# Kernel optimization log

Hardware: AMD Instinct MI355X
Metric: run time of the kernel (lower is better)

## Reference

```python
import jax, jax.numpy as jnp
import numpy as np

N, B, T, E = 16384, 8, 32, 262144
D, H = 256, 8
HD = D // H

def _ln(x, g, b, eps=1e-5):
    m = x.mean(-1, keepdims=True)
    va = x.var(-1, keepdims=True)
    return (x - m) * jax.lax.rsqrt(va + eps) * g + b

def setup_inputs():
    key = jax.random.key(0)
    ks = jax.random.split(key, 40)
    rn = lambda i, sh, s=0.02: jax.random.normal(ks[i], sh, jnp.float32) * s
    inp = {}
    inp['x'] = jax.random.normal(ks[0], (N, D), jnp.float32)
    inp['edge_index'] = jax.random.randint(ks[1], (2, E), 0, N)
    inp['edge_attr'] = jax.random.normal(ks[2], (E, D), jnp.float32)
    inp['v'] = jax.random.normal(ks[3], (B, T, D), jnp.float32)
    inp['batch'] = jnp.sort(jax.random.randint(ks[4], (N,), 0, B))
    ones = lambda sh: jnp.ones(sh, jnp.float32)
    zeros = lambda sh: jnp.zeros(sh, jnp.float32)
    # LayerNorms
    inp['n1_g'], inp['n1_b'] = ones((D,)), zeros((D,))
    inp['vn_g'], inp['vn_b'] = ones((D,)), zeros((D,))
    inp['n3_g'], inp['n3_b'] = ones((D,)), zeros((D,))
    inp['n4_g'], inp['n4_b'] = ones((D,)), zeros((D,))
    # GINEConv: eps (train_eps, init 0) + MLP [D, 2D, D] with layer_norm+gelu on hidden
    inp['gine_eps'] = jnp.float32(0.0)
    inp['g_w1'], inp['g_b1'] = rn(5, (2 * D, D)), zeros((2 * D,))
    inp['g_lng'], inp['g_lnb'] = ones((2 * D,)), zeros((2 * D,))
    inp['g_w2'], inp['g_b2'] = rn(6, (D, 2 * D)), zeros((D,))
    # GatedResidual gammas (init 1e-5)
    inp['gamma1'] = jnp.full((D,), 1e-5, jnp.float32)
    inp['gamma2'] = jnp.full((D,), 1e-5, jnp.float32)
    inp['gamma3'] = jnp.full((D,), 1e-5, jnp.float32)
    # MultiheadAttention (packed in_proj)
    inp['mha_in_w'], inp['mha_in_b'] = rn(7, (3 * D, D)), zeros((3 * D,))
    inp['mha_out_w'], inp['mha_out_b'] = rn(8, (D, D)), zeros((D,))
    # node->token cross attention projections
    inp['q_w'], inp['q_b'] = rn(9, (D, D)), zeros((D,))
    inp['kv_w'], inp['kv_b'] = rn(10, (2 * D, D)), zeros((2 * D,))
    inp['o_w'], inp['o_b'] = rn(11, (D, D)), zeros((D,))
    # FFN MLP [D, 4D, D] (eval-mode batch_norm == identity with default stats)
    inp['f_w1'], inp['f_b1'] = rn(12, (4 * D, D)), zeros((4 * D,))
    inp['f_w2'], inp['f_b2'] = rn(13, (D, 4 * D)), zeros((D,))
    return inp

def reference(x, edge_index, edge_attr, v, batch,
              n1_g, n1_b, vn_g, vn_b, n3_g, n3_b, n4_g, n4_b,
              gine_eps, g_w1, g_b1, g_lng, g_lnb, g_w2, g_b2,
              gamma1, gamma2, gamma3,
              mha_in_w, mha_in_b, mha_out_w, mha_out_b,
              q_w, q_b, kv_w, kv_b, o_w, o_b,
              f_w1, f_b1, f_w2, f_b2):
    scale = HD ** -0.5
    gelu = lambda t: jax.nn.gelu(t, approximate=False)
    # --- GINEConv on norm1(x) ---
    xn = _ln(x, n1_g, n1_b)
    src, dst = edge_index[0], edge_index[1]
    msg = jax.nn.relu(xn[src] + edge_attr)                      # [E, D]
    agg = jax.ops.segment_sum(msg, dst, num_segments=N)         # [N, D]
    hin = (1.0 + gine_eps) * xn + agg
    h = gelu(_ln(hin @ g_w1.T + g_b1, g_lng, g_lnb)) @ g_w2.T + g_b2
    x = x + gamma1 * h                                          # res1 (drop_path off in eval)
    # --- token self-attention with node summary context ---
    v_res = v
    vn = _ln(v, vn_g, vn_b)
    cnt = jnp.maximum(jax.ops.segment_sum(jnp.ones((N,), x.dtype), batch, num_segments=B), 1.0)
    node_summary = jax.ops.segment_sum(x, batch, num_segments=B) / cnt[:, None]  # [B, D]
    ctx = jnp.concatenate([vn, node_summary[:, None, :]], axis=1)                # [B, T+1, D]
    wq, wk, wv = jnp.split(mha_in_w, 3, axis=0)
    bq, bk, bv = jnp.split(mha_in_b, 3, axis=0)
    qh = (vn @ wq.T + bq).reshape(B, T, H, HD)
    kh = (ctx @ wk.T + bk).reshape(B, T + 1, H, HD)
    vh = (ctx @ wv.T + bv).reshape(B, T + 1, H, HD)
    a = jax.nn.softmax(jnp.einsum('bqhd,bkhd->bhqk', qh, kh) * scale, axis=-1)
    v_upd = jnp.einsum('bhqk,bkhd->bqhd', a, vh).reshape(B, T, D) @ mha_out_w.T + mha_out_b
    v = v_res + gamma2 * v_upd                                  # res2
    # --- node -> token cross attention (gather-expand KV by batch) ---
    xn3 = _ln(x, n3_g, n3_b)
    q = (xn3 @ q_w.T + q_b).reshape(N, H, HD)
    kv = (v @ kv_w.T + kv_b).reshape(B, T, 2, H, HD)
    k, val = kv[:, :, 0], kv[:, :, 1]                           # [B, T, H, HD]
    k_exp, val_exp = k[batch], val[batch]                       # [N, T, H, HD]
    scores = jnp.einsum('nhd,nthd->nht', q, k_exp) * scale
    attn = jax.nn.softmax(scores, axis=-1)                      # scatter_softmax w/ all-zero idx == softmax over t
    attn_out = jnp.einsum('nht,nthd->nhd', attn, val_exp).reshape(N, D)
    x = x + gamma3 * (attn_out @ o_w.T + o_b)                   # res3
    # --- FFN ---
    xn4 = _ln(x, n4_g, n4_b)
    x = x + (gelu(xn4 @ f_w1.T + f_b1) @ f_w2.T + f_b2)
    return (x, v)
```

## Files before the change

kernel.cpp:

```cpp
#include <hip/hip_runtime.h>
#include <math.h>

#define NN 16384
#define EE 262144
#define BB 8
#define TT 32
#define DD 256
#define HH 8
#define HDD 32

typedef __bf16 bf16;
typedef __bf16 bf16x8 __attribute__((ext_vector_type(8)));
typedef __bf16 bf16x4 __attribute__((ext_vector_type(4)));
typedef float f32x4 __attribute__((ext_vector_type(4)));

#define GM_F32 0
#define GM_BF16 1
#define GM_GELU 2
#define GM_RES 3
#define GM_RES2 4

__device__ __forceinline__ float gelu_f(float v) {
  return 0.5f * v * (1.f + erff(v * 0.70710678118654752440f));
}

__device__ __forceinline__ void ln256w(const float* __restrict__ xr,
                                       const float* __restrict__ g,
                                       const float* __restrict__ bb,
                                       bf16* __restrict__ o) {
  int lane = threadIdx.x & 63;
  float4 v = *(const float4*)(xr + lane * 4);
  float s = v.x + v.y + v.z + v.w;
  float s2 = v.x * v.x + v.y * v.y + v.z * v.z + v.w * v.w;
#pragma unroll
  for (int off = 32; off > 0; off >>= 1) {
    s += __shfl_xor(s, off, 64);
    s2 += __shfl_xor(s2, off, 64);
  }
  float m = s * (1.f / 256.f);
  float rs = rsqrtf(s2 * (1.f / 256.f) - m * m + 1e-5f);
  float4 gg = *(const float4*)(g + lane * 4);
  float4 bv = *(const float4*)(bb + lane * 4);
  bf16x4 ov;
  ov[0] = (bf16)((v.x - m) * rs * gg.x + bv.x);
  ov[1] = (bf16)((v.y - m) * rs * gg.y + bv.y);
  ov[2] = (bf16)((v.z - m) * rs * gg.z + bv.z);
  ov[3] = (bf16)((v.w - m) * rs * gg.w + bv.w);
  *(bf16x4*)(o + lane * 4) = ov;
}

struct Pro {
  const float* wsrc[9];
  bf16* wdst[9];
// ... 38 lines not shown
  }
}

__global__ __launch_bounds__(1024) void scan16k(const int* __restrict__ deg,
                                                int* __restrict__ offs, int* __restrict__ woff) {
  __shared__ int part[1024];
  int t = threadIdx.x;
  int base = t * 16;
  int v[16];
  int s = 0;
#pragma unroll
  for (int j = 0; j < 16; ++j) { v[j] = deg[base + j]; s += v[j]; }
  part[t] = s;
  __syncthreads();
  for (int o = 1; o < 1024; o <<= 1) {
    int x = (t >= o) ? part[t - o] : 0;
    __syncthreads();
    part[t] += x;
    __syncthreads();
  }
  int excl = part[t] - s;
#pragma unroll
  for (int j = 0; j < 16; ++j) {
    offs[base + j] = excl;
    woff[base + j] = excl;
    excl += v[j];
  }
  if (t == 1023) offs[NN] = part[1023];
}

struct GemmP {
  const bf16* A; const bf16* W; const float* bias;
  int M, K, NC, mode;
  const float* res; const float* gamma;
  float* outf; bf16* outb;
};

__device__ __forceinline__ void gemm_core(const GemmP p, int bx, int by) {
  int wave = threadIdx.x >> 6;
  int lane = threadIdx.x & 63;
  int qd = lane >> 4;
  int l16 = lane & 15;
  int r0 = by * 128 + wave * 32;
  int c0 = bx * 64;
  int ar0 = r0 + l16;       if (ar0 >= p.M) ar0 = p.M - 1;
  int ar1 = r0 + 16 + l16;  if (ar1 >= p.M) ar1 = p.M - 1;
  const bf16* Ap0 = p.A + (size_t)ar0 * p.K + qd * 8;
  const bf16* Ap1 = p.A + (size_t)ar1 * p.K + qd * 8;
  const bf16* Wp = p.W + (size_t)(c0 + l16) * p.K + qd * 8;
  size_t K16 = (size_t)16 * p.K;
  f32x4 acc00 = {0.f, 0.f, 0.f, 0.f};
  f32x4 acc01 = acc00, acc02 = acc00, acc03 = acc00;
  f32x4 acc10 = acc00, acc11 = acc00, acc12 = acc00, acc13 = acc00;
  bf16x8 a0, a1, b0, b1, b2, b3, na0, na1, nb0, nb1, nb2, nb3;

#define GLOADS(A0, A1, B0, B1, B2, B3, kk)                \
  A0 = *(const bf16x8*)(Ap0 + (kk));                      \
  A1 = *(const bf16x8*)(Ap1 + (kk));                      \
  B0 = *(const bf16x8*)(Wp + (kk));                       \
  B1 = *(const bf16x8*)(Wp + K16 + (kk));                 \
  B2 = *(const bf16x8*)(Wp + 2 * K16 + (kk));             \
  B3 = *(const bf16x8*)(Wp + 3 * K16 + (kk));
#define GMFMAS(A0, A1, B0, B1, B2, B3)                                  \
  acc00 = __builtin_amdgcn_mfma_f32_16x16x32_bf16(A0, B0, acc00, 0, 0, 0); \
  acc01 = __builtin_amdgcn_mfma_f32_16x16x32_bf16(A0, B1, acc01, 0, 0, 0); \
  acc02 = __builtin_amdgcn_mfma_f32_16x16x32_bf16(A0, B2, acc02, 0, 0, 0); \
  acc03 = __builtin_amdgcn_mfma_f32_16x16x32_bf16(A0, B3, acc03, 0, 0, 0); \
  acc10 = __builtin_amdgcn_mfma_f32_16x16x32_bf16(A1, B0, acc10, 0, 0, 0); \
  acc11 = __builtin_amdgcn_mfma_f32_16x16x32_bf16(A1, B1, acc11, 0, 0, 0); \
  acc12 = __builtin_amdgcn_mfma_f32_16x16x32_bf16(A1, B2, acc12, 0, 0, 0); \
  acc13 = __builtin_amdgcn_mfma_f32_16x16x32_bf16(A1, B3, acc13, 0, 0, 0);

  GLOADS(a0, a1, b0, b1, b2, b3, 0)
  int k = 32;
  for (; k + 32 < p.K; k += 64) {
    GLOADS(na0, na1, nb0, nb1, nb2, nb3, k)
    GMFMAS(a0, a1, b0, b1, b2, b3)
    GLOADS(a0, a1, b0, b1, b2, b3, k + 32)
    GMFMAS(na0, na1, nb0, nb1, nb2, nb3)
  }
  GLOADS(na0, na1, nb0, nb1, nb2, nb3, k)
  GMFMAS(a0, a1, b0, b1, b2, b3)
  GMFMAS(na0, na1, nb0, nb1, nb2, nb3)
#undef GLOADS
#undef GMFMAS

  f32x4 accs[2][4] = {{acc00, acc01, acc02, acc03}, {acc10, acc11, acc12, acc13}};
#pragma unroll
  for (int s = 0; s < 2; ++s) {
#pragma unroll
    for (int c = 0; c < 4; ++c) {
      int col = c0 + c * 16 + l16;
      float bv = p.bias[col];
#pragma unroll
      for (int i = 0; i < 4; ++i) {
        int row = r0 + s * 16 + qd * 4 + i;
        if (row >= p.M) continue;
        size_t idx = (size_t)row * p.NC + col;
        float v = accs[s][c][i] + bv;
        if (p.mode == GM_F32) p.outf[idx] = v;
        else if (p.mode == GM_BF16) p.outb[idx] = (bf16)v;
        else if (p.mode == GM_GELU) p.outb[idx] = (bf16)gelu_f(v);
        else {
          float g = p.gamma ? p.gamma[col] : 1.f;
          float r = p.res[idx] + g * v;
          p.outf[idx] = r;
          if (p.mode == GM_RES2) p.outb[idx] = (bf16)r;
        }
      }
    }
  }
}

__global__ __launch_bounds__(256) void gemm_one(GemmP p, int nbx) {
  gemm_core(p, blockIdx.x % nbx, blockIdx.x / nbx);
}

__global__ __launch_bounds__(256) void csr_fill_qh(const int* __restrict__ ei,
                                                   int* __restrict__ woff,
                                                   int2* __restrict__ csr2, GemmP qp) {
  int b = blockIdx.x;
  if (b < 1024) {
    int e = b * 256 + threadIdx.x;
    int d = ei[EE + e];
    int s = ei[e];
    int p = atomicAdd(&woff[d], 1);
    csr2[p] = make_int2(e, s);
  } else {
    int l = b - 1024;
    gemm_core(qp, l % 4, l / 4);
  }
}

__global__ __launch_bounds__(256) void gine_agg(const float* __restrict__ eattr,
                                                const bf16* __restrict__ xn,
                                                const int* __restrict__ offs,
                                                const int2* __restrict__ csr2,
                                                const float* __restrict__ epsp,
                                                bf16* __restrict__ hin) {
  int wave = threadIdx.x >> 6, lane = threadIdx.x & 63;
  int n = blockIdx.x * 4 + wave;
  int s0 = offs[n], s1 = offs[n + 1];
  f32x4 acc = {0.f, 0.f, 0.f, 0.f};
  int i = s0;
  int2 es = (i < s1) ? csr2[i] : make_int2(0, 0);
  for (; i < s1; ++i) {
    int2 cur = es;
    if (i + 1 < s1) es = csr2[i + 1];
    float4 ea = *(const float4*)(eattr + (size_t)cur.x * DD + lane * 4);
    bf16x4 xv = *(const bf16x4*)(xn + (size_t)cur.y * DD + lane * 4);
    acc[0] += fmaxf((float)xv[0] + ea.x, 0.f);
    acc[1] += fmaxf((float)xv[1] + ea.y, 0.f);
    acc[2] += fmaxf((float)xv[2] + ea.z, 0.f);
    acc[3] += fmaxf((float)xv[3] + ea.w, 0.f);
  }
  bf16x4 xs = *(const bf16x4*)(xn + (size_t)n * DD + lane * 4);
  float e1 = 1.f + epsp[0];
  bf16x4 o;
#pragma unroll
  for (int j = 0; j < 4; ++j)
    o[j] = (bf16)(e1 * (float)xs[j] + acc[j]);
  *(bf16x4*)(hin + (size_t)n * DD + lane * 4) = o;
}

__global__ __launch_bounds__(256) void gemm_g1_ln(const bf16* __restrict__ A,
                                                  const bf16* __restrict__ W,
                                                  const float* __restrict__ bias,
                                                  const float* __restrict__ lng,
                                                  const float* __restrict__ lnb,
                                                  bf16* __restrict__ out) {
  __shared__ float ssum[4][32], ssum2[4][32], smm[32], smr[32];
  int w = threadIdx.x >> 6, lane = threadIdx.x & 63;
  int qd = lane >> 4, l16 = lane & 15;
  int r0 = blockIdx.x * 32;
  int c0 = w * 128;
  const bf16* Ap0 = A + (size_t)(r0 + l16) * 256 + qd * 8;
  const bf16* Ap1 = Ap0 + (size_t)16 * 256;
  const bf16* Wp = W + (size_t)(c0 + l16) * 256 + qd * 8;
  f32x4 z = {0.f, 0.f, 0.f, 0.f};
  f32x4 acc0[8], acc1[8];
#pragma unroll
  for (int cf = 0; cf < 8; ++cf) { acc0[cf] = z; acc1[cf] = z; }
  for (int k = 0; k < 256; k += 32) {
    bf16x8 a0 = *(const bf16x8*)(Ap0 + k);
    bf16x8 a1 = *(const bf16x8*)(Ap1 + k);
#pragma unroll
    for (int cf = 0; cf < 8; ++cf) {
      bf16x8 bv = *(const bf16x8*)(Wp + (size_t)cf * 16 * 256 + k);
      acc0[cf] = __builtin_amdgcn_mfma_f32_16x16x32_bf16(a0, bv, acc0[cf], 0, 0, 0);
      acc1[cf] = __builtin_amdgcn_mfma_f32_16x16x32_bf16(a1, bv, acc1[cf], 0, 0, 0);
    }
  }
#pragma unroll
  for (int cf = 0; cf < 8; ++cf) {
    float bv = bias[c0 + cf * 16 + l16];
#pragma unroll
    for (int i = 0; i < 4; ++i) { acc0[cf][i] += bv; acc1[cf][i] += bv; }
  }
#pragma unroll
  for (int s = 0; s < 2; ++s) {
#pragma unroll
    for (int i = 0; i < 4; ++i) {
      float ps = 0.f, ps2 = 0.f;
#pragma unroll
      for (int cf = 0; cf < 8; ++cf) {
        float v = s ? acc1[cf][i] : acc0[cf][i];
        ps += v; ps2 += v * v;
      }
#pragma unroll
      for (int off = 8; off > 0; off >>= 1) {
        ps += __shfl_down(ps, off, 16);
        ps2 += __shfl_down(ps2, off, 16);
      }
      if (l16 == 0) { int rib = s * 16 + qd * 4 + i; ssum[w][rib] = ps; ssum2[w][rib] = ps2; }
    }
  }
  __syncthreads();
  if (threadIdx.x < 32) {
    int rib = threadIdx.x;
    float S = ssum[0][rib] + ssum[1][rib] + ssum[2][rib] + ssum[3][rib];
    float S2 = ssum2[0][rib] + ssum2[1][rib] + ssum2[2][rib] + ssum2[3][rib];
    float m = S * (1.f / 512.f);
    smm[rib] = m;
    smr[rib] = rsqrtf(S2 * (1.f / 512.f) - m * m + 1e-5f);
  }
  __syncthreads();
#pragma unroll
  for (int s = 0; s < 2; ++s) {
#pragma unroll
    for (int cf = 0; cf < 8; ++cf) {
      int col = c0 + cf * 16 + l16;
      float g = lng[col], b = lnb[col];
#pragma unroll
      for (int i = 0; i < 4; ++i) {
        int rib = s * 16 + qd * 4 + i;
        float v = ((s ? acc1[cf][i] : acc0[cf][i]) - smm[rib]) * smr[rib] * g + b;
        out[(size_t)(r0 + rib) * 512 + col] = (bf16)gelu_f(v);
      }
    }
  }
}

struct ResLnP {
  const bf16* A; const bf16* W; const float* bias;
  const float* res; const float* gamma;
  float* resout; const float* lng; const float* lnb; bf16* lnout;
  int K; int seg; const int* batch; float* summary;
};

__global__ __launch_bounds__(256) void gemm_res_ln(ResLnP p) {
  __shared__ float ssum[4][32], ssum2[4][32], smm[32], smr[32];
  int w = threadIdx.x >> 6, lane = threadIdx.x & 63;
  int qd = lane >> 4, l16 = lane & 15;
  int r0 = blockIdx.x * 32;
  int c0 = w * 64;
  const bf16* Ap0 = p.A + (size_t)(r0 + l16) * p.K + qd * 8;
  const bf16* Ap1 = Ap0 + (size_t)16 * p.K;
  const bf16* Wp = p.W + (size_t)(c0 + l16) * p.K + qd * 8;
  size_t K16 = (size_t)16 * p.K;
  f32x4 z = {0.f, 0.f, 0.f, 0.f};
  f32x4 acc0[4], acc1[4];
#pragma unroll
  for (int cf = 0; cf < 4; ++cf) { acc0[cf] = z; acc1[cf] = z; }
  for (int k = 0; k < p.K; k += 32) {
    bf16x8 a0 = *(const bf16x8*)(Ap0 + k);
    bf16x8 a1 = *(const bf16x8*)(Ap1 + k);
#pragma unroll
    for (int cf = 0; cf < 4; ++cf) {
      bf16x8 bv = *(const bf16x8*)(Wp + cf * K16 + k);
      acc0[cf] = __builtin_amdgcn_mfma_f32_16x16x32_bf16(a0, bv, acc0[cf], 0, 0, 0);
      acc1[cf] = __builtin_amdgcn_mfma_f32_16x16x32_bf16(a1, bv, acc1[cf], 0, 0, 0);
    }
  }
  float rr0[4][4], rr1[4][4];
#pragma unroll
  for (int cf = 0; cf < 4; ++cf) {
    int col = c0 + cf * 16 + l16;
    float bv = p.bias[col], gm = p.gamma[col];
#pragma unroll
    for (int i = 0; i < 4; ++i) {
// ... 24 lines not shown
#pragma unroll
      for (int off = 8; off > 0; off >>= 1) {
        ps += __shfl_down(ps, off, 16);
        ps2 += __shfl_down(ps2, off, 16);
      }
      if (l16 == 0) { int rib = s * 16 + qd * 4 + i; ssum[w][rib] = ps; ssum2[w][rib] = ps2; }
    }
  }
  __syncthreads();
  if (threadIdx.x < 32) {
    int rib = threadIdx.x;
    float S = ssum[0][rib] + ssum[1][rib] + ssum[2][rib] + ssum[3][rib];
    float S2 = ssum2[0][rib] + ssum2[1][rib] + ssum2[2][rib] + ssum2[3][rib];
    float m = S * (1.f / 256.f);
    smm[rib] = m;
    smr[rib] = rsqrtf(S2 * (1.f / 256.f) - m * m + 1e-5f);
  }
  __syncthreads();
#pragma unroll
  for (int cf = 0; cf < 4; ++cf) {
    int col = c0 + cf * 16 + l16;
    float lg = p.lng[col], lb = p.lnb[col];
#pragma unroll
    for (int i = 0; i < 4; ++i) {
      {
        int rib = qd * 4 + i;
        p.lnout[(size_t)(r0 + rib) * 256 + col] =
            (bf16)((rr0[cf][i] - smm[rib]) * smr[rib] * lg + lb);
      }
      {
        int rib = 16 + qd * 4 + i;
        p.lnout[(size_t)(r0 + rib) * 256 + col] =
            (bf16)((rr1[cf][i] - smm[rib]) * smr[rib] * lg + lb);
      }
    }
  }
  if (p.seg) {
    int b0 = p.batch[r0], b31 = p.batch[r0 + 31];
    if (b0 == b31) {
#pragma unroll
      for (int cf = 0; cf < 4; ++cf) {
        float sl = 0.f;
#pragma unroll
        for (int i = 0; i < 4; ++i) sl += rr0[cf][i] + rr1[cf][i];
        sl += __shfl_xor(sl, 16, 64);
        sl += __shfl_xor(sl, 32, 64);
        if (qd == 0) atomicAdd(&p.summary[(size_t)b0 * 256 + c0 + cf * 16 + l16], sl);
      }
    } else {
#pragma unroll
      for (int cf = 0; cf < 4; ++cf) {
        int col = c0 + cf * 16 + l16;
#pragma unroll
        for (int i = 0; i < 4; ++i) {
          atomicAdd(&p.summary[(size_t)p.batch[r0 + qd * 4 + i] * 256 + col], rr0[cf][i]);
          atomicAdd(&p.summary[(size_t)p.batch[r0 + 16 + qd * 4 + i] * 256 + col], rr1[cf][i]);
        }
      }
    }
  }
}

__global__ __launch_bounds__(256) void gemm_ffn(const bf16* __restrict__ A,
                                                const bf16* __restrict__ W1,
                                                const float* __restrict__ b1,
                                                const bf16* __restrict__ W2,
                                                const float* __restrict__ b2,
                                                const float* __restrict__ res,
                                                float* __restrict__ outx) {
  __shared__ bf16 t_lds[32 * 1032];
  int w = threadIdx.x >> 6, lane = threadIdx.x & 63;
  int qd = lane >> 4, l16 = lane & 15;
  int r0 = blockIdx.x * 32;
  {
    int c0 = w * 256;
    const bf16* Ap0 = A + (size_t)(r0 + l16) * 256 + qd * 8;
    const bf16* Ap1 = Ap0 + (size_t)16 * 256;
    const bf16* Wp = W1 + (size_t)(c0 + l16) * 256 + qd * 8;
    f32x4 z = {0.f, 0.f, 0.f, 0.f};
    f32x4 acc0[16], acc1[16];
#pragma unroll
    for (int cf = 0; cf < 16; ++cf) { acc0[cf] = z; acc1[cf] = z; }
    for (int k = 0; k < 256; k += 32) {
      bf16x8 a0 = *(const bf16x8*)(Ap0 + k);
      bf16x8 a1 = *(const bf16x8*)(Ap1 + k);
#pragma unroll
      for (int cf = 0; cf < 16; ++cf) {
        bf16x8 bv = *(const bf16x8*)(Wp + (size_t)cf * 16 * 256 + k);
        acc0[cf] = __builtin_amdgcn_mfma_f32_16x16x32_bf16(a0, bv, acc0[cf], 0, 0, 0);
        acc1[cf] = __builtin_amdgcn_mfma_f32_16x16x32_bf16(a1, bv, acc1[cf], 0, 0, 0);
// ... 16 lines not shown
    int c2 = w * 64;
    const bf16* Wp2 = W2 + (size_t)(c2 + l16) * 1024 + qd * 8;
    const bf16* lp0 = t_lds + l16 * 1032 + qd * 8;
    const bf16* lp1 = t_lds + (16 + l16) * 1032 + qd * 8;
    f32x4 z = {0.f, 0.f, 0.f, 0.f};
    f32x4 acc0[4], acc1[4];
#pragma unroll
    for (int cf = 0; cf < 4; ++cf) { acc0[cf] = z; acc1[cf] = z; }
    for (int k = 0; k < 1024; k += 32) {
      bf16x8 a0 = *(const bf16x8*)(lp0 + k);
      bf16x8 a1 = *(const bf16x8*)(lp1 + k);
#pragma unroll
      for (int cf = 0; cf < 4; ++cf) {
        bf16x8 bv = *(const bf16x8*)(Wp2 + (size_t)cf * 16 * 1024 + k);
        acc0[cf] = __builtin_amdgcn_mfma_f32_16x16x32_bf16(a0, bv, acc0[cf], 0, 0, 0);
        acc1[cf] = __builtin_amdgcn_mfma_f32_16x16x32_bf16(a1, bv, acc1[cf], 0, 0, 0);
      }
    }
#pragma unroll
    for (int cf = 0; cf < 4; ++cf) {
      int col = c2 + cf * 16 + l16;
      float bv = b2[col];
#pragma unroll
      for (int i = 0; i < 4; ++i) {
        int row0 = r0 + qd * 4 + i, row1 = row0 + 16;
        size_t i0 = (size_t)row0 * 256 + col, i1 = (size_t)row1 * 256 + col;
        outx[i0] = res[i0] + acc0[cf][i] + bv;
        outx[i1] = res[i1] + acc1[cf][i] + bv;
      }
    }
  }
}

__global__ __launch_bounds__(256) void mid2(const float* __restrict__ summary,
                                            const float* __restrict__ cntf,
                                            const bf16* __restrict__ vn,
                                            bf16* __restrict__ ctx,
                                            GemmP qp) {
  int b = blockIdx.x, t = threadIdx.x;
  if (b < BB * (TT + 1)) {
    int bb = b / (TT + 1), k = b % (TT + 1);
    float val;
    if (k < TT) val = (float)vn[((size_t)(bb * TT + k)) * DD + t];
    else val = summary[(size_t)bb * DD + t] / fmaxf(cntf[bb], 1.f);
    ctx[(size_t)b * DD + t] = (bf16)val;
  } else {
    int l = b - BB * (TT + 1);
    gemm_core(qp, l % 4, l / 4);
  }
}

__global__ __launch_bounds__(256) void mha_small(const float* __restrict__ qh,
                                                 const float* __restrict__ kvh,
                                                 bf16* __restrict__ vatt) {
  int b = blockIdx.x;
  int h = threadIdx.x >> 5, qi = threadIdx.x & 31;
  const float scale = 0.17677669529663687f;
  float sc[TT + 1];
  float mx = -1e30f;
  const float* qp = qh + ((size_t)(b * TT + qi)) * DD + h * HDD;
#pragma unroll
  for (int k = 0; k < TT + 1; ++k) {
    const float* kp = kvh + ((size_t)(b * (TT + 1) + k)) * 512 + h * HDD;
    float s = 0.f;
#pragma unroll
    for (int d = 0; d < HDD; ++d) s += qp[d] * kp[d];
    s *= scale;
    sc[k] = s;
    mx = fmaxf(mx, s);
  }
  float sum = 0.f;
#pragma unroll
  for (int k = 0; k < TT + 1; ++k) {
    sc[k] = __expf(sc[k] - mx);
    sum += sc[k];
  }
  float inv = 1.f / sum;
#pragma unroll
  for (int d = 0; d < HDD; ++d) {
    float o = 0.f;
#pragma unroll
    for (int k = 0; k < TT + 1; ++k)
      o += sc[k] * kvh[((size_t)(b * (TT + 1) + k)) * 512 + 256 + h * HDD + d];
    vatt[((size_t)(b * TT + qi)) * DD + h * HDD + d] = (bf16)(o * inv);
  }
}

__global__ __launch_bounds__(256) void cross_attn(const bf16* __restrict__ qx,
                                                  const float* __restrict__ kvx,
                                                  const int* __restrict__ batch,
                                                  bf16* __restrict__ attnout) {
  __shared__ float v_lds[TT * DD];
  int tid = threadIdx.x;
  int n0 = blockIdx.x * 16;
  int b0 = batch[n0];
  for (int i = tid; i < TT * DD; i += 256) {
    int t = i >> 8, c = i & 255;
    v_lds[i] = kvx[((size_t)(b0 * TT + t)) * 512 + 256 + c];
  }
  int h = tid >> 5, lt = tid & 31;
  float kreg[HDD];
  {
    const float* kp = kvx + ((size_t)(b0 * TT + lt)) * 512 + h * HDD;
#pragma unroll
    for (int d = 0; d < HDD; ++d) kreg[d] = kp[d];
  }
  __syncthreads();
  const float scale = 0.17677669529663687f;
  for (int ni = 0; ni < 16; ++ni) {
    int n = n0 + ni;
    int b = batch[n];
    const bf16* qp = qx + (size_t)n * DD + h * HDD;
    float s = 0.f;
    if (b == b0) {
#pragma unroll
      for (int d = 0; d < HDD; ++d) s += (float)qp[d] * kreg[d];
    } else {
// ... 67 lines not shown
  const float* o_b = (const float*)d_in[32];
  const float* f_w1 = (const float*)d_in[33];
  const float* f_b1 = (const float*)d_in[34];
  const float* f_w2 = (const float*)d_in[35];
  const float* f_b2 = (const float*)d_in[36];

  float* out_x = (float*)d_out;
  float* out_v = (float*)d_out + (size_t)NN * DD;

  char* wsp = (char*)d_ws;
  size_t off = 0;
  auto alloc = [&](size_t bytes) -> void* {
    void* p = wsp + off;
    off += (bytes + 255) & ~(size_t)255;
    return p;
  };
  float* t1f = (float*)alloc(33554432);
  bf16* xn_bf = (bf16*)alloc(8388608);
  bf16* qx_bf = xn_bf;
  bf16* t1g_bf = (bf16*)alloc(16777216);
  float* x2f = (float*)t1g_bf;
  float* x1f = (float*)alloc(16777216);
  bf16* hin_bf = (bf16*)alloc(8388608);
  bf16* xn3_bf = hin_bf;
  bf16* att_bf = (bf16*)alloc(8388608);
  bf16* xn4_bf = att_bf;
  int* deg = (int*)alloc(NN * 4);
  float* summary = (float*)alloc(BB * DD * 4);
  float* cntf = (float*)alloc(BB * 4);
  int* offs = (int*)alloc((NN + 1) * 4);
  int* woff = (int*)alloc(NN * 4);
  int2* csr2 = (int2*)alloc((size_t)EE * 8);
  bf16* vn_bf = (bf16*)alloc(BB * TT * DD * 2);
  bf16* ctx_bf = (bf16*)alloc(BB * (TT + 1) * DD * 2);
  float* qhf = (float*)alloc(BB * TT * DD * 4);
  float* kvhf = (float*)alloc(BB * (TT + 1) * 512 * 4);
  bf16* vatt_bf = (bf16*)alloc(BB * TT * DD * 2);
  bf16* vout_bf = (bf16*)alloc(BB * TT * DD * 2);
  float* kvxf = (float*)alloc(BB * TT * 512 * 4);
  bf16* wbuf = (bf16*)alloc((size_t)1310720 * 2);
  (void)t1f;

  bf16* g_w1b = wbuf;
  bf16* g_w2b = g_w1b + 131072;
  bf16* mha_in_wb = g_w2b + 131072;
  bf16* q_wb = mha_in_wb + 196608;
  bf16* kv_wb = q_wb + 65536;
  bf16* o_wb = kv_wb + 131072;
  bf16* f_w1b = o_wb + 65536;
  bf16* f_w2b = f_w1b + 262144;
  bf16* mha_out_wb = f_w2b + 262144;

  hipMemsetAsync(deg, 0, NN * 4 + BB * DD * 4 + 256, stream);

  Pro pr;
  pr.wsrc[0] = g_w1; pr.wdst[0] = g_w1b;
  pr.wsrc[1] = g_w2; pr.wdst[1] = g_w2b;
  pr.wsrc[2] = mha_in_w; pr.wdst[2] = mha_in_wb;
  pr.wsrc[3] = mha_out_w; pr.wdst[3] = mha_out_wb;
  pr.wsrc[4] = q_w; pr.wdst[4] = q_wb;
  pr.wsrc[5] = kv_w; pr.wdst[5] = kv_wb;
  pr.wsrc[6] = o_w; pr.wdst[6] = o_wb;
  pr.wsrc[7] = f_w1; pr.wdst[7] = f_w1b;
  pr.wsrc[8] = f_w2; pr.wdst[8] = f_w2b;
  int bs[10] = {0, 128, 256, 448, 512, 576, 704, 768, 1024, 1280};
  for (int i = 0; i < 10; ++i) pr.wblk[i] = bs[i];
  pr.x = x; pr.n1_g = n1_g; pr.n1_b = n1_b; pr.xn = xn_bf;
  pr.v = v; pr.vn_g = vn_g; pr.vn_b = vn_b; pr.vn = vn_bf;
  pr.batch = batch; pr.cntf = cntf;
  pr.ei = ei; pr.deg = deg;
  prologue<<<6528, 256, 0, stream>>>(pr);

  scan16k<<<1, 1024, 0, stream>>>(deg, offs, woff);

  GemmP j_qh = {vn_bf, mha_in_wb, mha_in_b, BB * TT, 256, 256, GM_F32,
                nullptr, nullptr, qhf, nullptr};
  csr_fill_qh<<<1024 + 8, 256, 0, stream>>>(ei, woff, csr2, j_qh);

  gine_agg<<<NN / 4, 256, 0, stream>>>(eattr, xn_bf, offs, csr2, gine_eps, hin_bf);

  gemm_g1_ln<<<NN / 32, 256, 0, stream>>>(hin_bf, g_w1b, g_b1, g_lng, g_lnb, t1g_bf);

  ResLnP j_g2 = {t1g_bf, g_w2b, g_b2, x, gamma1, x1f, n3_g, n3_b, xn3_bf,
                 512, 1, batch, summary};
  gemm_res_ln<<<NN / 32, 256, 0, stream>>>(j_g2);

  GemmP j_q = {xn3_bf, q_wb, q_b, NN, 256, 256, GM_BF16, nullptr, nullptr, nullptr, qx_bf};
  mid2<<<BB * (TT + 1) + 512, 256, 0, stream>>>(summary, cntf, vn_bf, ctx_bf, j_q);

  GemmP j_kvh = {ctx_bf, mha_in_wb + (size_t)256 * 256, mha_in_b + 256, BB * (TT + 1), 256, 512,
                 GM_F32, nullptr, nullptr, kvhf, nullptr};
  gemm_one<<<24, 256, 0, stream>>>(j_kvh, 8);

  mha_small<<<BB, 256, 0, stream>>>(qhf, kvhf, vatt_bf);

  GemmP j_mo = {vatt_bf, mha_out_wb, mha_out_b, BB * TT, 256, 256, GM_RES2, v, gamma2, out_v, vout_bf};
  gemm_one<<<8, 256, 0, stream>>>(j_mo, 4);

  GemmP j_kv = {vout_bf, kv_wb, kv_b, BB * TT, 256, 512, GM_F32, nullptr, nullptr, kvxf, nullptr};
  gemm_one<<<16, 256, 0, stream>>>(j_kv, 8);

  cross_attn<<<NN / 16, 256, 0, stream>>>(qx_bf, kvxf, batch, att_bf);

  ResLnP j_o = {att_bf, o_wb, o_b, x1f, gamma3, x2f, n4_g, n4_b, xn4_bf,
                256, 0, nullptr, nullptr};
  gemm_res_ln<<<NN / 32, 256, 0, stream>>>(j_o);

  gemm_ffn<<<NN / 32, 256, 0, stream>>>(xn4_bf, f_w1b, f_b1, f_w2b, f_b2, x2f, out_x);
}
```

Baseline: 888.7 us.

## Fuse GINE MLP GEMMs via LDS and collapse token-side chain into one kernel

The two GINE MLP GEMMs (with hidden LayerNorm+GELU, then the residual, norm3 and segment-sum epilogue) are fused into one kernel. The 512-wide hidden activation stays in shared memory instead of round-tripping through global memory. The token-side chain (ctx build, KV projection, small MHA, out-projection with residual, KV projection for cross attention) is fused into 8 blocks that run alongside the node Q-projection GEMM blocks in one launch. This cuts several launches and intermediate buffers, at the cost of large LDS use per block, which may reduce occupancy. The csr_fill blocks are also reordered so the small GEMM blocks launch first.

```diff
diff --git a/kernel.cpp b/kernel.cpp
--- a/kernel.cpp
+++ b/kernel.cpp
@@ -16,9 +16,6 @@
 
 #define GM_F32 0
 #define GM_BF16 1
-#define GM_GELU 2
-#define GM_RES 3
-#define GM_RES2 4
 
 __device__ __forceinline__ float gelu_f(float v) {
   return 0.5f * v * (1.f + erff(v * 0.70710678118654752440f));
@@ -123,7 +120,6 @@
 struct GemmP {
   const bf16* A; const bf16* W; const float* bias;
   int M, K, NC, mode;
-  const float* res; const float* gamma;
   float* outf; bf16* outb;
 };
 
@@ -190,36 +186,24 @@
         size_t idx = (size_t)row * p.NC + col;
         float v = accs[s][c][i] + bv;
         if (p.mode == GM_F32) p.outf[idx] = v;
-        else if (p.mode == GM_BF16) p.outb[idx] = (bf16)v;
-        else if (p.mode == GM_GELU) p.outb[idx] = (bf16)gelu_f(v);
-        else {
-          float g = p.gamma ? p.gamma[col] : 1.f;
-          float r = p.res[idx] + g * v;
-          p.outf[idx] = r;
-          if (p.mode == GM_RES2) p.outb[idx] = (bf16)r;
-        }
-      }
-    }
-  }
-}
-
-__global__ __launch_bounds__(256) void gemm_one(GemmP p, int nbx) {
-  gemm_core(p, blockIdx.x % nbx, blockIdx.x / nbx);
+        else p.outb[idx] = (bf16)v;
+      }
+    }
+  }
 }
 
 __global__ __launch_bounds__(256) void csr_fill_qh(const int* __restrict__ ei,
                                                    int* __restrict__ woff,
                                                    int2* __restrict__ csr2, GemmP qp) {
   int b = blockIdx.x;
-  if (b < 1024) {
-    int e = b * 256 + threadIdx.x;
+  if (b < 8) {
+    gemm_core(qp, b % 4, b / 4);
+  } else {
+    int e = (b - 8) * 256 + threadIdx.x;
     int d = ei[EE + e];
     int s = ei[e];
     int p = atomicAdd(&woff[d], 1);
     csr2[p] = make_int2(e, s);
-  } else {
-    int l = b - 1024;
-    gemm_core(qp, l % 4, l / 4);
   }
 }
 
@@ -254,79 +238,197 @@
   *(bf16x4*)(hin + (size_t)n * DD + lane * 4) = o;
 }
 
-__global__ __launch_bounds__(256) void gemm_g1_ln(const bf16* __restrict__ A,
-                                                  const bf16* __restrict__ W,
-                                                  const float* __restrict__ bias,
-                                                  const float* __restrict__ lng,
-                                                  const float* __restrict__ lnb,
-                                                  bf16* __restrict__ out) {
+struct G12P {
+  const bf16* A; const bf16* W1; const float* b1;
+  const float* lng; const float* lnb;
+  const bf16* W2; const float* b2;
+  const float* res; const float* gamma;
+  float* resout; const float* n3g; const float* n3b; bf16* xn3;
+  const int* batch; float* summary;
+};
+
+__global__ __launch_bounds__(256) void gemm_g1g2(G12P p) {
+  __shared__ bf16 t_l[32 * 520];
   __shared__ float ssum[4][32], ssum2[4][32], smm[32], smr[32];
   int w = threadIdx.x >> 6, lane = threadIdx.x & 63;
   int qd = lane >> 4, l16 = lane & 15;
   int r0 = blockIdx.x * 32;
-  int c0 = w * 128;
-  const bf16* Ap0 = A + (size_t)(r0 + l16) * 256 + qd * 8;
-  const bf16* Ap1 = Ap0 + (size_t)16 * 256;
-  const bf16* Wp = W + (size_t)(c0 + l16) * 256 + qd * 8;
-  f32x4 z = {0.f, 0.f, 0.f, 0.f};
-  f32x4 acc0[8], acc1[8];
-#pragma unroll
-  for (int cf = 0; cf < 8; ++cf) { acc0[cf] = z; acc1[cf] = z; }
-  for (int k = 0; k < 256; k += 32) {
-    bf16x8 a0 = *(const bf16x8*)(Ap0 + k);
-    bf16x8 a1 = *(const bf16x8*)(Ap1 + k);
+  {
+    int c0 = w * 128;
+    const bf16* Ap0 = p.A + (size_t)(r0 + l16) * 256 + qd * 8;
+    const bf16* Ap1 = Ap0 + (size_t)16 * 256;
+    const bf16* Wp = p.W1 + (size_t)(c0 + l16) * 256 + qd * 8;
+    f32x4 z = {0.f, 0.f, 0.f, 0.f};
+    f32x4 acc0[8], acc1[8];
+#pragma unroll
+    for (int cf = 0; cf < 8; ++cf) { acc0[cf] = z; acc1[cf] = z; }
+    for (int k = 0; k < 256; k += 32) {
+      bf16x8 a0 = *(const bf16x8*)(Ap0 + k);
+      bf16x8 a1 = *(const bf16x8*)(Ap1 + k);
+#pragma unroll
+      for (int cf = 0; cf < 8; ++cf) {
+        bf16x8 bv = *(const bf16x8*)(Wp + (size_t)cf * 16 * 256 + k);
+        acc0[cf] = __builtin_amdgcn_mfma_f32_16x16x32_bf16(a0, bv, acc0[cf], 0, 0, 0);
+        acc1[cf] = __builtin_amdgcn_mfma_f32_16x16x32_bf16(a1, bv, acc1[cf], 0, 0, 0);
+      }
+    }
 #pragma unroll
     for (int cf = 0; cf < 8; ++cf) {
-      bf16x8 bv = *(const bf16x8*)(Wp + (size_t)cf * 16 * 256 + k);
-      acc0[cf] = __builtin_amdgcn_mfma_f32_16x16x32_bf16(a0, bv, acc0[cf], 0, 0, 0);
-      acc1[cf] = __builtin_amdgcn_mfma_f32_16x16x32_bf16(a1, bv, acc1[cf], 0, 0, 0);
-    }
-  }
-#pragma unroll
-  for (int cf = 0; cf < 8; ++cf) {
-    float bv = bias[c0 + cf * 16 + l16];
-#pragma unroll
-    for (int i = 0; i < 4; ++i) { acc0[cf][i] += bv; acc1[cf][i] += bv; }
-  }
-#pragma unroll
-  for (int s = 0; s < 2; ++s) {
-#pragma unroll
-    for (int i = 0; i < 4; ++i) {
-      float ps = 0.f, ps2 = 0.f;
+      float bv = p.b1[c0 + cf * 16 + l16];
+#pragma unroll
+      for (int i = 0; i < 4; ++i) { acc0[cf][i] += bv; acc1[cf][i] += bv; }
+    }
+#pragma unroll
+    for (int s = 0; s < 2; ++s) {
+#pragma unroll
+      for (int i = 0; i < 4; ++i) {
+        float ps = 0.f, ps2 = 0.f;
+#pragma unroll
+        for (int cf = 0; cf < 8; ++cf) {
+          float v = s ? acc1[cf][i] : acc0[cf][i];
+          ps += v; ps2 += v * v;
+        }
+#pragma unroll
+        for (int off = 8; off > 0; off >>= 1) {
+          ps += __shfl_down(ps, off, 16);
+          ps2 += __shfl_down(ps2, off, 16);
+        }
+        if (l16 == 0) { int rib = s * 16 + qd * 4 + i; ssum[w][rib] = ps; ssum2[w][rib] = ps2; }
+      }
+    }
+    __syncthreads();
+    if (threadIdx.x < 32) {
+      int rib = threadIdx.x;
+      float S = ssum[0][rib] + ssum[1][rib] + ssum[2][rib] + ssum[3][rib];
+      float S2 = ssum2[0][rib] + ssum2[1][rib] + ssum2[2][rib] + ssum2[3][rib];
+      float m = S * (1.f / 512.f);
+      smm[rib] = m;
+      smr[rib] = rsqrtf(S2 * (1.f / 512.f) - m * m + 1e-5f);
+    }
+    __syncthreads();
+#pragma unroll
+    for (int s = 0; s < 2; ++s) {
 #pragma unroll
       for (int cf = 0; cf < 8; ++cf) {
-        float v = s ? acc1[cf][i] : acc0[cf][i];
-        ps += v; ps2 += v * v;
-      }
-#pragma unroll
-      for (int off = 8; off > 0; off >>= 1) {
-        ps += __shfl_down(ps, off, 16);
-        ps2 += __shfl_down(ps2, off, 16);
-      }
-      if (l16 == 0) { int rib = s * 16 + qd * 4 + i; ssum[w][rib] = ps; ssum2[w][rib] = ps2; }
+        int col = c0 + cf * 16 + l16;
+        float g = p.lng[col], b = p.lnb[col];
+#pragma unroll
+        for (int i = 0; i < 4; ++i) {
+          int rib = s * 16 + qd * 4 + i;
+          float v = ((s ? acc1[cf][i] : acc0[cf][i]) - smm[rib]) * smr[rib] * g + b;
+          t_l[rib * 520 + col] = (bf16)gelu_f(v);
+        }
+      }
     }
   }
   __syncthreads();
-  if (threadIdx.x < 32) {
-    int rib = threadIdx.x;
-    float S = ssum[0][rib] + ssum[1][rib] + ssum[2][rib] + ssum[3][rib];
-    float S2 = ssum2[0][rib] + ssum2[1][rib] + ssum2[2][rib] + ssum2[3][rib];
-    float m = S * (1.f / 512.f);
-    smm[rib] = m;
-    smr[rib] = rsqrtf(S2 * (1.f / 512.f) - m * m + 1e-5f);
-  }
-  __syncthreads();
-#pragma unroll
-  for (int s = 0; s < 2; ++s) {
-#pragma unroll
-    for (int cf = 0; cf < 8; ++cf) {
+  {
+    int c0 = w * 64;
+    const bf16* lp0 = t_l + l16 * 520 + qd * 8;
+    const bf16* lp1 = t_l + (16 + l16) * 520 + qd * 8;
+    const bf16* Wp = p.W2 + (size_t)(c0 + l16) * 512 + qd * 8;
+    f32x4 z = {0.f, 0.f, 0.f, 0.f};
+    f32x4 acc0[4], acc1[4];
+#pragma unroll
+    for (int cf = 0; cf < 4; ++cf) { acc0[cf] = z; acc1[cf] = z; }
+    for (int k = 0; k < 512; k += 32) {
+      bf16x8 a0 = *(const bf16x8*)(lp0 + k);
+      bf16x8 a1 = *(const bf16x8*)(lp1 + k);
+#pragma unroll
+      for (int cf = 0; cf < 4; ++cf) {
+        bf16x8 bv = *(const bf16x8*)(Wp + (size_t)cf * 16 * 512 + k);
+        acc0[cf] = __builtin_amdgcn_mfma_f32_16x16x32_bf16(a0, bv, acc0[cf], 0, 0, 0);
+        acc1[cf] = __builtin_amdgcn_mfma_f32_16x16x32_bf16(a1, bv, acc1[cf], 0, 0, 0);
+      }
+    }
+    float rr0[4][4], rr1[4][4];
+#pragma unroll
+    for (int cf = 0; cf < 4; ++cf) {
       int col = c0 + cf * 16 + l16;
-      float g = lng[col], b = lnb[col];
+      float bv = p.b2[col], gm = p.gamma[col];
 #pragma unroll
       for (int i = 0; i < 4; ++i) {
-        int rib = s * 16 + qd * 4 + i;
-        float v = ((s ? acc1[cf][i] : acc0[cf][i]) - smm[rib]) * smr[rib] * g + b;
-        out[(size_t)(r0 + rib) * 512 + col] = (bf16)gelu_f(v);
+        {
+          int row = r0 + qd * 4 + i;
+          size_t idx = (size_t)row * 256 + col;
+          float r = p.res[idx] + gm * (acc0[cf][i] + bv);
+          p.resout[idx] = r; rr0[cf][i] = r;
+        }
+        {
+          int row = r0 + 16 + qd * 4 + i;
+          size_t idx = (size_t)row * 256 + col;
+          float r = p.res[idx] + gm * (acc1[cf][i] + bv);
+          p.resout[idx] = r; rr1[cf][i] = r;
+        }
+      }
+    }
+    __syncthreads();
+#pragma unroll
+    for (int s = 0; s < 2; ++s) {
+#pragma unroll
+      for (int i = 0; i < 4; ++i) {
+        float ps = 0.f, ps2 = 0.f;
+#pragma unroll
+        for (int cf = 0; cf < 4; ++cf) {
+          float v = s ? rr1[cf][i] : rr0[cf][i];
+          ps += v; ps2 += v * v;
+        }
+#pragma unroll
+        for (int off = 8; off > 0; off >>= 1) {
+          ps += __shfl_down(ps, off, 16);
+          ps2 += __shfl_down(ps2, off, 16);
+        }
+        if (l16 == 0) { int rib = s * 16 + qd * 4 + i; ssum[w][rib] = ps; ssum2[w][rib] = ps2; }
+      }
+    }
+    __syncthreads();
+    if (threadIdx.x < 32) {
+      int rib = threadIdx.x;
+      float S = ssum[0][rib] + ssum[1][rib] + ssum[2][rib] + ssum[3][rib];
+      float S2 = ssum2[0][rib] + ssum2[1][rib] + ssum2[2][rib] + ssum2[3][rib];
+      float m = S * (1.f / 256.f);
+      smm[rib] = m;
+      smr[rib] = rsqrtf(S2 * (1.f / 256.f) - m * m + 1e-5f);
+    }
+    __syncthreads();
+#pragma unroll
+    for (int cf = 0; cf < 4; ++cf) {
+      int col = c0 + cf * 16 + l16;
+      float lg = p.n3g[col], lb = p.n3b[col];
+#pragma unroll
+      for (int i = 0; i < 4; ++i) {
+        {
+          int rib = qd * 4 + i;
+          p.xn3[(size_t)(r0 + rib) * 256 + col] =
+              (bf16)((rr0[cf][i] - smm[rib]) * smr[rib] * lg + lb);
+        }
+        {
+          int rib = 16 + qd * 4 + i;
+          p.xn3[(size_t)(r0 + rib) * 256 + col] =
+              (bf16)((rr1[cf][i] - smm[rib]) * smr[rib] * lg + lb);
+        }
+      }
+    }
+    int b0 = p.batch[r0], b31 = p.batch[r0 + 31];
+    if (b0 == b31) {
+#pragma unroll
+      for (int cf = 0; cf < 4; ++cf) {
+        float sl = 0.f;
+#pragma unroll
+        for (int i = 0; i < 4; ++i) sl += rr0[cf][i] + rr1[cf][i];
+        sl += __shfl_xor(sl, 16, 64);
+        sl += __shfl_xor(sl, 32, 64);
+        if (qd == 0) atomicAdd(&p.summary[(size_t)b0 * 256 + c0 + cf * 16 + l16], sl);
+      }
+    } else {
+#pragma unroll
+      for (int cf = 0; cf < 4; ++cf) {
+        int col = c0 + cf * 16 + l16;
+#pragma unroll
+        for (int i = 0; i < 4; ++i) {
+          atomicAdd(&p.summary[(size_t)p.batch[r0 + qd * 4 + i] * 256 + col], rr0[cf][i]);
+          atomicAdd(&p.summary[(size_t)p.batch[r0 + 16 + qd * 4 + i] * 256 + col], rr1[cf][i]);
+        }
       }
     }
   }
@@ -336,7 +438,7 @@
   const bf16* A; const bf16* W; const float* bias;
   const float* res; const float* gamma;
   float* resout; const float* lng; const float* lnb; bf16* lnout;
-  int K; int seg; const int* batch; float* summary;
+  int K;
 };
 
 __global__ __launch_bounds__(256) void gemm_res_ln(ResLnP p) {
@@ -427,30 +529,6 @@
         int rib = 16 + qd * 4 + i;
         p.lnout[(size_t)(r0 + rib) * 256 + col] =
             (bf16)((rr1[cf][i] - smm[rib]) * smr[rib] * lg + lb);
-      }
-    }
-  }
-  if (p.seg) {
-    int b0 = p.batch[r0], b31 = p.batch[r0 + 31];
-    if (b0 == b31) {
-#pragma unroll
-      for (int cf = 0; cf < 4; ++cf) {
-        float sl = 0.f;
-#pragma unroll
-        for (int i = 0; i < 4; ++i) sl += rr0[cf][i] + rr1[cf][i];
-        sl += __shfl_xor(sl, 16, 64);
-        sl += __shfl_xor(sl, 32, 64);
-        if (qd == 0) atomicAdd(&p.summary[(size_t)b0 * 256 + c0 + cf * 16 + l16], sl);
-      }
-    } else {
-#pragma unroll
-      for (int cf = 0; cf < 4; ++cf) {
-        int col = c0 + cf * 16 + l16;
-#pragma unroll
-        for (int i = 0; i < 4; ++i) {
-          atomicAdd(&p.summary[(size_t)p.batch[r0 + qd * 4 + i] * 256 + col], rr0[cf][i]);
-          atomicAdd(&p.summary[(size_t)p.batch[r0 + 16 + qd * 4 + i] * 256 + col], rr1[cf][i]);
-        }
       }
     }
   }
@@ -533,57 +611,202 @@
   }
 }
 
-__global__ __launch_bounds__(256) void mid2(const float* __restrict__ summary,
-                                            const float* __restrict__ cntf,
-                                            const bf16* __restrict__ vn,
-                                            bf16* __restrict__ ctx,
-                                            GemmP qp) {
-  int b = blockIdx.x, t = threadIdx.x;
-  if (b < BB * (TT + 1)) {
-    int bb = b / (TT + 1), k = b % (TT + 1);
-    float val;
-    if (k < TT) val = (float)vn[((size_t)(bb * TT + k)) * DD + t];
-    else val = summary[(size_t)bb * DD + t] / fmaxf(cntf[bb], 1.f);
-    ctx[(size_t)b * DD + t] = (bf16)val;
-  } else {
-    int l = b - BB * (TT + 1);
+struct VtP {
+  const bf16* vn; const float* summary; const float* cntf; const float* qh;
+  const bf16* wkv_in; const float* bkv_in;
+  const bf16* wmo; const float* bmo;
+  const float* vres; const float* gamma2; float* outv;
+  const bf16* wkv2; const float* bkv2; float* kvx;
+};
+
+__global__ __launch_bounds__(256) void q_vtail(GemmP qp, VtP vt) {
+  __shared__ bf16 sl[25928];
+  int blk = blockIdx.x;
+  if (blk >= 8) {
+    int l = blk - 8;
     gemm_core(qp, l % 4, l / 4);
-  }
-}
-
-__global__ __launch_bounds__(256) void mha_small(const float* __restrict__ qh,
-                                                 const float* __restrict__ kvh,
-                                                 bf16* __restrict__ vatt) {
-  int b = blockIdx.x;
-  int h = threadIdx.x >> 5, qi = threadIdx.x & 31;
+    return;
+  }
+  int bb = blk;
+  int t = threadIdx.x;
+  int w = t >> 6, lane = t & 63, qd = lane >> 4, l16 = lane & 15;
+  bf16* ctx_l = sl;
+  bf16* kvh_l = sl + 8768;
+  bf16* vatt_l = sl;
+  bf16* vout_l = sl + 8768;
   const float scale = 0.17677669529663687f;
-  float sc[TT + 1];
-  float mx = -1e30f;
-  const float* qp = qh + ((size_t)(b * TT + qi)) * DD + h * HDD;
-#pragma unroll
-  for (int k = 0; k < TT + 1; ++k) {
-    const float* kp = kvh + ((size_t)(b * (TT + 1) + k)) * 512 + h * HDD;
-    float s = 0.f;
-#pragma unroll
-    for (int d = 0; d < HDD; ++d) s += qp[d] * kp[d];
-    s *= scale;
-    sc[k] = s;
-    mx = fmaxf(mx, s);
-  }
-  float sum = 0.f;
-#pragma unroll
-  for (int k = 0; k < TT + 1; ++k) {
-    sc[k] = __expf(sc[k] - mx);
-    sum += sc[k];
-  }
-  float inv = 1.f / sum;
-#pragma unroll
-  for (int d = 0; d < HDD; ++d) {
-    float o = 0.f;
-#pragma unroll
-    for (int k = 0; k < TT + 1; ++k)
-      o += sc[k] * kvh[((size_t)(b * (TT + 1) + k)) * 512 + 256 + h * HDD + d];
-    vatt[((size_t)(b * TT + qi)) * DD + h * HDD + d] = (bf16)(o * inv);
+
+  {
+    float cinv = 1.f / fmaxf(vt.cntf[bb], 1.f);
+    for (int r = 0; r < 33; ++r) {
+      float val;
+      if (r < 32) val = (float)vt.vn[((size_t)(bb * 32 + r)) * 256 + t];
+      else val = vt.summary[(size_t)bb * 256 + t] * cinv;
+      ctx_l[r * 264 + t] = (bf16)val;
+    }
+  }
+  __syncthreads();
+
+  {
+    const bf16* a0p = ctx_l + (l16 < 32 ? l16 : 32) * 264 + qd * 8;
+    const bf16* a1p = ctx_l + ((16 + l16) < 32 ? (16 + l16) : 32) * 264 + qd * 8;
+    const bf16* a2p = ctx_l + 32 * 264 + qd * 8;
+#pragma unroll
+    for (int sc = 0; sc < 2; ++sc) {
+      int c0 = w * 128 + sc * 64;
+      const bf16* Wp = vt.wkv_in + (size_t)(c0 + l16) * 256 + qd * 8;
+      f32x4 z = {0.f, 0.f, 0.f, 0.f};
+      f32x4 acc[3][4];
+#pragma unroll
+      for (int rg = 0; rg < 3; ++rg)
+#pragma unroll
+        for (int cf = 0; cf < 4; ++cf) acc[rg][cf] = z;
+      for (int k = 0; k < 256; k += 32) {
+        bf16x8 av0 = *(const bf16x8*)(a0p + k);
+        bf16x8 av1 = *(const bf16x8*)(a1p + k);
+        bf16x8 av2 = *(const bf16x8*)(a2p + k);
+#pragma unroll
+        for (int cf = 0; cf < 4; ++cf) {
+          bf16x8 bv = *(const bf16x8*)(Wp + (size_t)cf * 16 * 256 + k);
+          acc[0][cf] = __builtin_amdgcn_mfma_f32_16x16x32_bf16(av0, bv, acc[0][cf], 0, 0, 0);
+          acc[1][cf] = __builtin_amdgcn_mfma_f32_16x16x32_bf16(av1, bv, acc[1][cf], 0, 0, 0);
+          acc[2][cf] = __builtin_amdgcn_mfma_f32_16x16x32_bf16(av2, bv, acc[2][cf], 0, 0, 0);
+        }
+      }
+#pragma unroll
+      for (int cf = 0; cf < 4; ++cf) {
+        int col = c0 + cf * 16 + l16;
+        float bv = vt.bkv_in[col];
+#pragma unroll
+        for (int rg = 0; rg < 3; ++rg) {
+#pragma unroll
+          for (int i = 0; i < 4; ++i) {
+            int row = rg * 16 + qd * 4 + i;
+            if (row < 33) kvh_l[row * 520 + col] = (bf16)(acc[rg][cf][i] + bv);
+          }
+        }
+      }
+    }
+  }
+  __syncthreads();
+
+  {
+    int h = t >> 5, qi = t & 31;
+    float qreg[HDD];
+    const float* qp = vt.qh + ((size_t)(bb * TT + qi)) * DD + h * HDD;
+#pragma unroll
+    for (int d = 0; d < HDD; ++d) qreg[d] = qp[d];
+    float sc[TT + 1];
+    float mx = -1e30f;
+#pragma unroll
+    for (int k = 0; k < TT + 1; ++k) {
+      float s = 0.f;
+#pragma unroll
+      for (int d = 0; d < HDD; ++d) s += qreg[d] * (float)kvh_l[k * 520 + h * HDD + d];
+      s *= scale;
+      sc[k] = s;
+      mx = fmaxf(mx, s);
+    }
+    float sum = 0.f;
+#pragma unroll
+    for (int k = 0; k < TT + 1; ++k) {
+      sc[k] = __expf(sc[k] - mx);
+      sum += sc[k];
+    }
+    float inv = 1.f / sum;
+#pragma unroll
+    for (int d = 0; d < HDD; ++d) {
+      float o = 0.f;
+#pragma unroll
+      for (int k = 0; k < TT + 1; ++k)
+        o += sc[k] * (float)kvh_l[k * 520 + 256 + h * HDD + d];
+      vatt_l[qi * 264 + h * HDD + d] = (bf16)(o * inv);
+    }
+  }
+  __syncthreads();
+
+  {
+    int c0 = w * 64;
+    const bf16* a0p = vatt_l + l16 * 264 + qd * 8;
+    const bf16* a1p = vatt_l + (16 + l16) * 264 + qd * 8;
+    const bf16* Wp = vt.wmo + (size_t)(c0 + l16) * 256 + qd * 8;
+    f32x4 z = {0.f, 0.f, 0.f, 0.f};
+    f32x4 acc0[4], acc1[4];
+#pragma unroll
+    for (int cf = 0; cf < 4; ++cf) { acc0[cf] = z; acc1[cf] = z; }
+    for (int k = 0; k < 256; k += 32) {
+      bf16x8 a0 = *(const bf16x8*)(a0p + k);
+      bf16x8 a1 = *(const bf16x8*)(a1p + k);
+#pragma unroll
+      for (int cf = 0; cf < 4; ++cf) {
+        bf16x8 bv = *(const bf16x8*)(Wp + (size_t)cf * 16 * 256 + k);
+        acc0[cf] = __builtin_amdgcn_mfma_f32_16x16x32_bf16(a0, bv, acc0[cf], 0, 0, 0);
+        acc1[cf] = __builtin_amdgcn_mfma_f32_16x16x32_bf16(a1, bv, acc1[cf], 0, 0, 0);
+      }
+    }
+#pragma unroll
+    for (int cf = 0; cf < 4; ++cf) {
+      int col = c0 + cf * 16 + l16;
+      float bv = vt.bmo[col], gm = vt.gamma2[col];
+#pragma unroll
+      for (int i = 0; i < 4; ++i) {
+        {
+          int row = qd * 4 + i;
+          size_t idx = (size_t)(bb * TT + row) * 256 + col;
+          float r = vt.vres[idx] + gm * (acc0[cf][i] + bv);
+          vt.outv[idx] = r;
+          vout_l[row * 264 + col] = (bf16)r;
+        }
+        {
+          int row = 16 + qd * 4 + i;
+          size_t idx = (size_t)(bb * TT + row) * 256 + col;
+          float r = vt.vres[idx] + gm * (acc1[cf][i] + bv);
+          vt.outv[idx] = r;
+          vout_l[row * 264 + col] = (bf16)r;
+        }
+      }
+    }
+  }
+  __syncthreads();
+
+  {
+    const bf16* a0p = vout_l + l16 * 264 + qd * 8;
+    const bf16* a1p = vout_l + (16 + l16) * 264 + qd * 8;
+#pragma unroll
+    for (int sc = 0; sc < 2; ++sc) {
+      int c0 = w * 128 + sc * 64;
+      const bf16* Wp = vt.wkv2 + (size_t)(c0 + l16) * 256 + qd * 8;
+      f32x4 z = {0.f, 0.f, 0.f, 0.f};
+      f32x4 acc0[4], acc1[4];
+#pragma unroll
+      for (int cf = 0; cf < 4; ++cf) { acc0[cf] = z; acc1[cf] = z; }
+      for (int k = 0; k < 256; k += 32) {
+        bf16x8 a0 = *(const bf16x8*)(a0p + k);
+        bf16x8 a1 = *(const bf16x8*)(a1p + k);
+#pragma unroll
+        for (int cf = 0; cf < 4; ++cf) {
+          bf16x8 bv = *(const bf16x8*)(Wp + (size_t)cf * 16 * 256 + k);
+          acc0[cf] = __builtin_amdgcn_mfma_f32_16x16x32_bf16(a0, bv, acc0[cf], 0, 0, 0);
+          acc1[cf] = __builtin_amdgcn_mfma_f32_16x16x32_bf16(a1, bv, acc1[cf], 0, 0, 0);
+        }
+      }
+#pragma unroll
+      for (int cf = 0; cf < 4; ++cf) {
+        int col = c0 + cf * 16 + l16;
+        float bv = vt.bkv2[col];
+#pragma unroll
+        for (int i = 0; i < 4; ++i) {
+          {
+            int row = qd * 4 + i;
+            vt.kvx[(size_t)(bb * TT + row) * 512 + col] = acc0[cf][i] + bv;
+          }
+          {
+            int row = 16 + qd * 4 + i;
+            vt.kvx[(size_t)(bb * TT + row) * 512 + col] = acc1[cf][i] + bv;
+          }
+        }
+      }
+    }
   }
 }
 
@@ -717,11 +940,7 @@
   int* woff = (int*)alloc(NN * 4);
   int2* csr2 = (int2*)alloc((size_t)EE * 8);
   bf16* vn_bf = (bf16*)alloc(BB * TT * DD * 2);
-  bf16* ctx_bf = (bf16*)alloc(BB * (TT + 1) * DD * 2);
   float* qhf = (float*)alloc(BB * TT * DD * 4);
-  float* kvhf = (float*)alloc(BB * (TT + 1) * 512 * 4);
-  bf16* vatt_bf = (bf16*)alloc(BB * TT * DD * 2);
-  bf16* vout_bf = (bf16*)alloc(BB * TT * DD * 2);
   float* kvxf = (float*)alloc(BB * TT * 512 * 4);
   bf16* wbuf = (bf16*)alloc((size_t)1310720 * 2);
   (void)t1f;
@@ -758,37 +977,27 @@
 
   scan16k<<<1, 1024, 0, stream>>>(deg, offs, woff);
 
-  GemmP j_qh = {vn_bf, mha_in_wb, mha_in_b, BB * TT, 256, 256, GM_F32,
-                nullptr, nullptr, qhf, nullptr};
+  GemmP j_qh = {vn_bf, mha_in_wb, mha_in_b, BB * TT, 256, 256, GM_F32, qhf, nullptr};
   csr_fill_qh<<<1024 + 8, 256, 0, stream>>>(ei, woff, csr2, j_qh);
 
   gine_agg<<<NN / 4, 256, 0, stream>>>(eattr, xn_bf, offs, csr2, gine_eps, hin_bf);
 
-  gemm_g1_ln<<<NN / 32, 256, 0, stream>>>(hin_bf, g_w1b, g_b1, g_lng, g_lnb, t1g_bf);
-
-  ResLnP j_g2 = {t1g_bf, g_w2b, g_b2, x, gamma1, x1f, n3_g, n3_b, xn3_bf,
-                 512, 1, batch, summary};
-  gemm_res_ln<<<NN / 32, 256, 0, stream>>>(j_g2);
-
-  GemmP j_q = {xn3_bf, q_wb, q_b, NN, 256, 256, GM_BF16, nullptr, nullptr, nullptr, qx_bf};
-  mid2<<<BB * (TT + 1) + 512, 256, 0, stream>>>(summary, cntf, vn_bf, ctx_bf, j_q);
-
-  GemmP j_kvh = {ctx_bf, mha_in_wb + (size_t)256 * 256, mha_in_b + 256, BB * (TT + 1), 256, 512,
-                 GM_F32, nullptr, nullptr, kvhf, nullptr};
-  gemm_one<<<24, 256, 0, stream>>>(j_kvh, 8);
-
-  mha_small<<<BB, 256, 0, stream>>>(qhf, kvhf, vatt_bf);
-
-  GemmP j_mo = {vatt_bf, mha_out_wb, mha_out_b, BB * TT, 256, 256, GM_RES2, v, gamma2, out_v, vout_bf};
-  gemm_one<<<8, 256, 0, stream>>>(j_mo, 4);
-
-  GemmP j_kv = {vout_bf, kv_wb, kv_b, BB * TT, 256, 512, GM_F32, nullptr, nullptr, kvxf, nullptr};
-  gemm_one<<<16, 256, 0, stream>>>(j_kv, 8);
+  G12P jg = {hin_bf, g_w1b, g_b1, g_lng, g_lnb, g_w2b, g_b2, x, gamma1,
+             x1f, n3_g, n3_b, xn3_bf, batch, summary};
+  gemm_g1g2<<<NN / 32, 256, 0, stream>>>(jg);
+
+  GemmP j_q = {xn3_bf, q_wb, q_b, NN, 256, 256, GM_BF16, nullptr, qx_bf};
+  VtP vt;
+  vt.vn = vn_bf; vt.summary = summary; vt.cntf = cntf; vt.qh = qhf;
+  vt.wkv_in = mha_in_wb + (size_t)256 * 256; vt.bkv_in = mha_in_b + 256;
+  vt.wmo = mha_out_wb; vt.bmo = mha_out_b;
+  vt.vres = v; vt.gamma2 = gamma2; vt.outv = out_v;
+  vt.wkv2 = kv_wb; vt.bkv2 = kv_b; vt.kvx = kvxf;
+  q_vtail<<<8 + 512, 256, 0, stream>>>(j_q, vt);
 
   cross_attn<<<NN / 16, 256, 0, stream>>>(qx_bf, kvxf, batch, att_bf);
 
-  ResLnP j_o = {att_bf, o_wb, o_b, x1f, gamma3, x2f, n4_g, n4_b, xn4_bf,
-                256, 0, nullptr, nullptr};
+  ResLnP j_o = {att_bf, o_wb, o_b, x1f, gamma3, x2f, n4_g, n4_b, xn4_bf, 256};
   gemm_res_ln<<<NN / 32, 256, 0, stream>>>(j_o);
 
   gemm_ffn<<<NN / 32, 256, 0, stream>>>(xn4_bf, f_w1b, f_b1, f_w2b, f_b2, x2f, out_x);
```

Result: faster. 852.2 us (-4.1%).
